# Performance work log

Measured on AMD Instinct MI355X. Metric: run time of the kernel, lower is better.

The kernel has to match this reference:

```python
import jax, jax.numpy as jnp
import numpy as np

RADIUS = 0.5
NEG_INF = -jnp.inf


def setup_inputs() -> dict:
    key = jax.random.key(0)
    ks = jax.random.split(key, 10)
    N_q, N_o, pos_dim, latent_dim = 2048, 2048, 3, 64
    enc_dim = 3 * pos_dim  # q_pos, o_pos, rel
    inp = {
        "h_obs": jax.random.normal(ks[0], (N_o, latent_dim), dtype=jnp.float32),
        "x_obs": jax.random.normal(ks[1], (N_o, latent_dim), dtype=jnp.float32),
        "pos_obs": jax.random.uniform(ks[2], (N_o, pos_dim), dtype=jnp.float32),
        "pos_query": jax.random.uniform(ks[3], (N_q, pos_dim), dtype=jnp.float32),
        # kernel_mlp: Linear(enc_dim->latent) + ReLU + Linear(latent->1)
        "W1": jax.random.normal(ks[4], (enc_dim, latent_dim), dtype=jnp.float32) / np.sqrt(enc_dim),
        "b1": jnp.zeros((latent_dim,), dtype=jnp.float32),
        "W2": jax.random.normal(ks[5], (latent_dim, 1), dtype=jnp.float32) / np.sqrt(latent_dim),
        "b2": jnp.zeros((1,), dtype=jnp.float32),
        # value_proj: Linear(latent->latent)
        "Wv": jax.random.normal(ks[6], (latent_dim, latent_dim), dtype=jnp.float32) / np.sqrt(latent_dim),
        "bv": jnp.zeros((latent_dim,), dtype=jnp.float32),
    }
    return inp


def reference(h_obs, x_obs, pos_obs, pos_query, W1, b1, W2, b2, Wv, bv):
    # rel: [N_q, N_o, pos_dim]
    rel = pos_query[:, None, :] - pos_obs[None, :, :]
    N_q, N_o, _ = rel.shape
    pos_q_exp = jnp.broadcast_to(pos_query[:, None, :], rel.shape)
    pos_o_exp = jnp.broadcast_to(pos_obs[None, :, :], rel.shape)
    kernel_input = jnp.concatenate([pos_q_exp, pos_o_exp, rel], axis=-1)  # [N_q, N_o, 3*pos_dim]
    # small pointwise MLP over all pairs
    hidden = jax.nn.relu(jnp.einsum('qoe,el->qol', kernel_input, W1) + b1)  # [N_q, N_o, latent]
    logits = jnp.einsum('qol,lk->qok', hidden, W2)[..., 0] + b2[0]          # [N_q, N_o]
    # radius mask
    dist = jnp.linalg.norm(rel, axis=-1)
    logits = jnp.where(dist > RADIUS, NEG_INF, logits)
    # softmax over observations (dim=1)
    weights = jax.nn.softmax(logits, axis=1)  # [N_q, N_o]
    v = h_obs @ Wv + bv                        # [N_o, latent]
    h_query = weights @ v                      # [N_q, latent]
    return h_query
```

## Files before the change

### kernel.cpp

```cpp
#include <hip/hip_runtime.h>

#define NQ 2048
#define NO 2048
#define NOC 32

constexpr size_t OFF_PH = 0;
constexpr size_t OFF_PS = (size_t)NOC * NQ * 64;

__global__ __launch_bounds__(256, 4) void gano_main(
    const float* __restrict__ h_obs,
    const float* __restrict__ pos_obs,
    const float* __restrict__ pos_query,
    const float* __restrict__ W1,
    const float* __restrict__ b1,
    const float* __restrict__ W2,
    float* __restrict__ Ph,
    float* __restrict__ Ps)
{
    __shared__ __align__(16) float tl[64 * 68];
    __shared__ __align__(16) float ue[16 * 64 * 4];
    __shared__ float w1q[3 * 64];
    __shared__ float w1o[3 * 64];
    __shared__ float b1l[64];
    __shared__ __align__(16) float w2l[64];
    __shared__ float po[3 * 64];
    __shared__ float sbuf[4 * 64];

    const int tid  = threadIdx.x;
    const int lane = tid & 63;
    const int wave = __builtin_amdgcn_readfirstlane(tid >> 6);
    const int qg = blockIdx.x >> 5;
    const int oc = blockIdx.x & 31;
    const int obase = oc * 64;
    const int q = qg * 64 + lane;

    if (tid < 64) {
        float w6 = W1[6 * 64 + tid], w7 = W1[7 * 64 + tid], w8 = W1[8 * 64 + tid];
        w1q[0 * 64 + tid] = W1[0 * 64 + tid] + w6;
        w1q[1 * 64 + tid] = W1[1 * 64 + tid] + w7;
        w1q[2 * 64 + tid] = W1[2 * 64 + tid] + w8;
        w1o[0 * 64 + tid] = W1[3 * 64 + tid] - w6;
        w1o[1 * 64 + tid] = W1[4 * 64 + tid] - w7;
        w1o[2 * 64 + tid] = W1[5 * 64 + tid] - w8;
        b1l[tid] = b1[tid];
        w2l[tid] = W2[tid];
    }
    float pq0 = pos_query[q * 3 + 0];
    float pq1 = pos_query[q * 3 + 1];
    float pq2 = pos_query[q * 3 + 2];
    float po0 = pos_obs[(obase + lane) * 3 + 0];
    float po1 = pos_obs[(obase + lane) * 3 + 1];
    float po2 = pos_obs[(obase + lane) * 3 + 2];
    if (wave == 0) { po[lane] = po0; po[64 + lane] = po1; po[128 + lane] = po2; }
    __syncthreads();

#pragma unroll
    for (int j = 0; j < 16; ++j) {
        int l = wave * 16 + j;
        tl[l * 68 + lane] = po0 * w1o[l] + po1 * w1o[64 + l] + po2 * w1o[128 + l];
    }
#pragma unroll
    for (int k = 0; k < 4; ++k) {
        int lb = wave * 4 + k;
        float4 uv;
        {
            int l = lb * 4;
            uv.x = b1l[l+0] + pq0 * w1q[l+0] + pq1 * w1q[64 + l+0] + pq2 * w1q[128 + l+0];
            uv.y = b1l[l+1] + pq0 * w1q[l+1] + pq1 * w1q[64 + l+1] + pq2 * w1q[128 + l+1];
            uv.z = b1l[l+2] + pq0 * w1q[l+2] + pq1 * w1q[64 + l+2] + pq2 * w1q[128 + l+2];
            uv.w = b1l[l+3] + pq0 * w1q[l+3] + pq1 * w1q[64 + l+3] + pq2 * w1q[128 + l+3];
        }
        *(float4*)(ue + (size_t)(lb * 64 + lane) * 4) = uv;
    }
    __syncthreads();

    float lg[16];
#pragma unroll
    for (int o = 0; o < 16; ++o) lg[o] = 0.f;
    const int ow = wave * 16;
#pragma unroll
    for (int lb = 0; lb < 16; ++lb) {
        float4 u4 = *(const float4*)(ue + (size_t)(lb * 64 + lane) * 4);
        float4 w4 = *(const float4*)(w2l + lb * 4);
#pragma unroll
        for (int dl = 0; dl < 4; ++dl) {
            const int l = lb * 4 + dl;
            const float4* tr = (const float4*)(tl + l * 68 + ow);
            float ul = (dl == 0) ? u4.x : (dl == 1) ? u4.y : (dl == 2) ? u4.z : u4.w;
            float wl = (dl == 0) ? w4.x : (dl == 1) ? w4.y : (dl == 2) ? w4.z : w4.w;
#pragma unroll
            for (int j = 0; j < 4; ++j) {
                float4 t4 = tr[j];
                lg[4 * j + 0] += wl * fmaxf(ul + t4.x, 0.f);
                lg[4 * j + 1] += wl * fmaxf(ul + t4.y, 0.f);
                lg[4 * j + 2] += wl * fmaxf(ul + t4.z, 0.f);
                lg[4 * j + 3] += wl * fmaxf(ul + t4.w, 0.f);
            }
        }
    }
    float e[16], spart = 0.f;
#pragma unroll
    for (int o = 0; o < 16; ++o) {
        float d0 = pq0 - po[ow + o];
        float d1 = pq1 - po[64 + ow + o];
        float d2 = pq2 - po[128 + ow + o];
        float dd = d0 * d0 + d1 * d1 + d2 * d2;
        float ev = (dd > 0.25f) ? 0.f : __expf(lg[o]);
        e[o] = ev; spart += ev;
    }
    __syncthreads();
#pragma unroll
    for (int o = 0; o < 16; ++o) ue[(size_t)(ow + o) * 64 + lane] = e[o];
    sbuf[wave * 64 + lane] = spart;
    __syncthreads();

    float h0 = 0.f, h1 = 0.f, h2 = 0.f, h3 = 0.f, h4 = 0.f, h5 = 0.f, h6 = 0.f, h7 = 0.f;
    float h8 = 0.f, h9 = 0.f, hA = 0.f, hB = 0.f, hC = 0.f, hD = 0.f, hE = 0.f, hF = 0.f;
    const float* vb = h_obs + (size_t)obase * 64 + ow;
#pragma unroll 4
    for (int o = 0; o < 64; ++o) {
        float eo = ue[(size_t)o * 64 + lane];
        const float4* vr = (const float4*)(vb + (size_t)o * 64);
        float4 v0 = vr[0], v1 = vr[1], v2 = vr[2], v3 = vr[3];
        h0 += eo * v0.x; h1 += eo * v0.y; h2 += eo * v0.z; h3 += eo * v0.w;
        h4 += eo * v1.x; h5 += eo * v1.y; h6 += eo * v1.z; h7 += eo * v1.w;
        h8 += eo * v2.x; h9 += eo * v2.y; hA += eo * v2.z; hB += eo * v2.w;
        hC += eo * v3.x; hD += eo * v3.y; hE += eo * v3.z; hF += eo * v3.w;
    }

    float* hp = Ph + ((size_t)oc * NQ + (size_t)qg * 64 + lane) * 64 + ow;
    ((float4*)hp)[0] = make_float4(h0, h1, h2, h3);
    ((float4*)hp)[1] = make_float4(h4, h5, h6, h7);
    ((float4*)hp)[2] = make_float4(h8, h9, hA, hB);
    ((float4*)hp)[3] = make_float4(hC, hD, hE, hF);
    if (wave == 0) {
        float s = sbuf[lane] + sbuf[64 + lane] + sbuf[128 + lane] + sbuf[192 + lane];
        Ps[(size_t)oc * NQ + (size_t)qg * 64 + lane] = s;
    }
}

__global__ __launch_bounds__(256, 2) void gano_comb(
    const float* __restrict__ Ph,
    const float* __restrict__ Ps,
    const float* __restrict__ Wv,
    const float* __restrict__ bv,
    float* __restrict__ out)
{
    __shared__ __align__(16) float wv[64 * 64];
    __shared__ __align__(16) float g[4 * 68];
    const int tid  = threadIdx.x;
    const int lane = tid & 63;
    const int wave = tid >> 6;
    const int q0 = blockIdx.x * 4;
    {
        const float4* src = (const float4*)Wv;
        float4* dst = (float4*)wv;
#pragma unroll
        for (int k = 0; k < 4; ++k) dst[tid + k * 256] = src[tid + k * 256];
    }
    {
        const int qi = wave, k = lane;
        float acc = 0.f;
#pragma unroll
        for (int c = 0; c < NOC; ++c)
            acc += Ph[((size_t)c * NQ + q0 + qi) * 64 + k];
        g[qi * 68 + k] = acc;
        if (k == 0) {
            float ss = 0.f;
#pragma unroll
            for (int c = 0; c < NOC; ++c) ss += Ps[(size_t)c * NQ + q0 + qi];
            g[qi * 68 + 64] = ss;
        }
    }
    __syncthreads();
    const float* gq = g + wave * 68;
    float inv = 1.0f / gq[64];
    float a0 = 0.f, a1 = 0.f, a2 = 0.f, a3 = 0.f;
#pragma unroll
    for (int kb = 0; kb < 16; ++kb) {
        float4 g4 = *(const float4*)(gq + kb * 4);
        a0 += g4.x * wv[(kb * 4 + 0) * 64 + lane];
        a1 += g4.y * wv[(kb * 4 + 1) * 64 + lane];
        a2 += g4.z * wv[(kb * 4 + 2) * 64 + lane];
        a3 += g4.w * wv[(kb * 4 + 3) * 64 + lane];
    }
    out[(size_t)(q0 + wave) * 64 + lane] = ((a0 + a1) + (a2 + a3)) * inv + bv[lane];
}

extern "C" void kernel_launch(void* const* d_in, const int* in_sizes, int n_in,
                              void* d_out, int out_size, void* d_ws, size_t ws_size,
                              hipStream_t stream) {
    const float* h_obs     = (const float*)d_in[0];
    const float* pos_obs   = (const float*)d_in[2];
    const float* pos_query = (const float*)d_in[3];
    const float* W1        = (const float*)d_in[4];
    const float* b1        = (const float*)d_in[5];
    const float* W2        = (const float*)d_in[6];
    const float* Wv        = (const float*)d_in[8];
    const float* bv        = (const float*)d_in[9];
    float* ws  = (float*)d_ws;
    float* out = (float*)d_out;

    gano_main<<<dim3(1024), dim3(256), 0, stream>>>(h_obs, pos_obs, pos_query, W1, b1, W2,
                                                    ws + OFF_PH, ws + OFF_PS);
    gano_comb<<<dim3(NQ / 4), dim3(256), 0, stream>>>(ws + OFF_PH, ws + OFF_PS, Wv, bv, out);
}
```

Measured before the change: 108.2 us.

## Precompute obs-side hidden term in prep kernel and read via scalar loads

Adds a prep kernel that computes the observation-side first-layer term T[o][l] once into workspace, instead of every block rebuilding it in LDS. The main kernel keeps the query-side hidden vector in 64 registers and reads T rows, W2, pos_obs and h_obs through wave-uniform (readfirstlane) addresses, so those loads can become scalar loads rather than LDS traffic. Most LDS staging and several barriers are removed. The costs are an extra kernel launch, much higher register pressure from the u[64] array, which may hurt occupancy under launch_bounds(256,4), and dependence on scalar-cache bandwidth.

```diff
diff --git a/kernel.cpp b/kernel.cpp
--- a/kernel.cpp
+++ b/kernel.cpp
@@ -4,10 +4,25 @@
 #define NO 2048
 #define NOC 32
 
-constexpr size_t OFF_PH = 0;
-constexpr size_t OFF_PS = (size_t)NOC * NQ * 64;
+constexpr size_t OFF_T  = 0;
+constexpr size_t OFF_PH = (size_t)NO * 64;
+constexpr size_t OFF_PS = OFF_PH + (size_t)NOC * NQ * 64;
+
+__global__ __launch_bounds__(256) void gano_prep(
+    const float* __restrict__ pos_obs,
+    const float* __restrict__ W1,
+    float* __restrict__ T)
+{
+    int gid = blockIdx.x * 256 + threadIdx.x;
+    int o = gid >> 6, l = gid & 63;
+    float po0 = pos_obs[o * 3 + 0], po1 = pos_obs[o * 3 + 1], po2 = pos_obs[o * 3 + 2];
+    float w3 = W1[3 * 64 + l], w4 = W1[4 * 64 + l], w5 = W1[5 * 64 + l];
+    float w6 = W1[6 * 64 + l], w7 = W1[7 * 64 + l], w8 = W1[8 * 64 + l];
+    T[(size_t)o * 64 + l] = po0 * (w3 - w6) + po1 * (w4 - w7) + po2 * (w5 - w8);
+}
 
 __global__ __launch_bounds__(256, 4) void gano_main(
+    const float* __restrict__ T,
     const float* __restrict__ h_obs,
     const float* __restrict__ pos_obs,
     const float* __restrict__ pos_query,
@@ -17,13 +32,7 @@
     float* __restrict__ Ph,
     float* __restrict__ Ps)
 {
-    __shared__ __align__(16) float tl[64 * 68];
-    __shared__ __align__(16) float ue[16 * 64 * 4];
-    __shared__ float w1q[3 * 64];
-    __shared__ float w1o[3 * 64];
-    __shared__ float b1l[64];
-    __shared__ __align__(16) float w2l[64];
-    __shared__ float po[3 * 64];
+    __shared__ float ue[64 * 64];
     __shared__ float sbuf[4 * 64];
 
     const int tid  = threadIdx.x;
@@ -32,100 +41,63 @@
     const int qg = blockIdx.x >> 5;
     const int oc = blockIdx.x & 31;
     const int obase = oc * 64;
-    const int q = qg * 64 + lane;
+    const int q  = qg * 64 + lane;
+    const int ow = wave * 16;
 
-    if (tid < 64) {
-        float w6 = W1[6 * 64 + tid], w7 = W1[7 * 64 + tid], w8 = W1[8 * 64 + tid];
-        w1q[0 * 64 + tid] = W1[0 * 64 + tid] + w6;
-        w1q[1 * 64 + tid] = W1[1 * 64 + tid] + w7;
-        w1q[2 * 64 + tid] = W1[2 * 64 + tid] + w8;
-        w1o[0 * 64 + tid] = W1[3 * 64 + tid] - w6;
-        w1o[1 * 64 + tid] = W1[4 * 64 + tid] - w7;
-        w1o[2 * 64 + tid] = W1[5 * 64 + tid] - w8;
-        b1l[tid] = b1[tid];
-        w2l[tid] = W2[tid];
-    }
     float pq0 = pos_query[q * 3 + 0];
     float pq1 = pos_query[q * 3 + 1];
     float pq2 = pos_query[q * 3 + 2];
-    float po0 = pos_obs[(obase + lane) * 3 + 0];
-    float po1 = pos_obs[(obase + lane) * 3 + 1];
-    float po2 = pos_obs[(obase + lane) * 3 + 2];
-    if (wave == 0) { po[lane] = po0; po[64 + lane] = po1; po[128 + lane] = po2; }
-    __syncthreads();
 
+    float u[64];
 #pragma unroll
-    for (int j = 0; j < 16; ++j) {
-        int l = wave * 16 + j;
-        tl[l * 68 + lane] = po0 * w1o[l] + po1 * w1o[64 + l] + po2 * w1o[128 + l];
+    for (int l = 0; l < 64; ++l) {
+        float a = b1[l];
+        a += pq0 * W1[0 * 64 + l];
+        a += pq1 * W1[1 * 64 + l];
+        a += pq2 * W1[2 * 64 + l];
+        a += pq0 * W1[6 * 64 + l];
+        a += pq1 * W1[7 * 64 + l];
+        a += pq2 * W1[8 * 64 + l];
+        u[l] = a;
     }
+
+    float spart = 0.f;
+#pragma unroll 2
+    for (int o = 0; o < 16; ++o) {
+        const int toff = __builtin_amdgcn_readfirstlane((obase + ow + o) * 64);
+        const float* __restrict__ trow = T + toff;
+        float a0 = 0.f, a1 = 0.f, a2 = 0.f, a3 = 0.f;
 #pragma unroll
-    for (int k = 0; k < 4; ++k) {
-        int lb = wave * 4 + k;
-        float4 uv;
-        {
-            int l = lb * 4;
-            uv.x = b1l[l+0] + pq0 * w1q[l+0] + pq1 * w1q[64 + l+0] + pq2 * w1q[128 + l+0];
-            uv.y = b1l[l+1] + pq0 * w1q[l+1] + pq1 * w1q[64 + l+1] + pq2 * w1q[128 + l+1];
-            uv.z = b1l[l+2] + pq0 * w1q[l+2] + pq1 * w1q[64 + l+2] + pq2 * w1q[128 + l+2];
-            uv.w = b1l[l+3] + pq0 * w1q[l+3] + pq1 * w1q[64 + l+3] + pq2 * w1q[128 + l+3];
+        for (int l = 0; l < 64; l += 4) {
+            a0 += W2[l + 0] * fmaxf(u[l + 0] + trow[l + 0], 0.f);
+            a1 += W2[l + 1] * fmaxf(u[l + 1] + trow[l + 1], 0.f);
+            a2 += W2[l + 2] * fmaxf(u[l + 2] + trow[l + 2], 0.f);
+            a3 += W2[l + 3] * fmaxf(u[l + 3] + trow[l + 3], 0.f);
         }
-        *(float4*)(ue + (size_t)(lb * 64 + lane) * 4) = uv;
+        float lgo = (a0 + a1) + (a2 + a3);
+        const int poff = __builtin_amdgcn_readfirstlane((obase + ow + o) * 3);
+        float d0 = pq0 - pos_obs[poff + 0];
+        float d1 = pq1 - pos_obs[poff + 1];
+        float d2 = pq2 - pos_obs[poff + 2];
+        float dd = d0 * d0 + d1 * d1 + d2 * d2;
+        float ev = (dd > 0.25f) ? 0.f : __expf(lgo);
+        spart += ev;
+        ue[(ow + o) * 64 + lane] = ev;
     }
-    __syncthreads();
-
-    float lg[16];
-#pragma unroll
-    for (int o = 0; o < 16; ++o) lg[o] = 0.f;
-    const int ow = wave * 16;
-#pragma unroll
-    for (int lb = 0; lb < 16; ++lb) {
-        float4 u4 = *(const float4*)(ue + (size_t)(lb * 64 + lane) * 4);
-        float4 w4 = *(const float4*)(w2l + lb * 4);
-#pragma unroll
-        for (int dl = 0; dl < 4; ++dl) {
-            const int l = lb * 4 + dl;
-            const float4* tr = (const float4*)(tl + l * 68 + ow);
-            float ul = (dl == 0) ? u4.x : (dl == 1) ? u4.y : (dl == 2) ? u4.z : u4.w;
-            float wl = (dl == 0) ? w4.x : (dl == 1) ? w4.y : (dl == 2) ? w4.z : w4.w;
-#pragma unroll
-            for (int j = 0; j < 4; ++j) {
-                float4 t4 = tr[j];
-                lg[4 * j + 0] += wl * fmaxf(ul + t4.x, 0.f);
-                lg[4 * j + 1] += wl * fmaxf(ul + t4.y, 0.f);
-                lg[4 * j + 2] += wl * fmaxf(ul + t4.z, 0.f);
-                lg[4 * j + 3] += wl * fmaxf(ul + t4.w, 0.f);
-            }
-        }
-    }
-    float e[16], spart = 0.f;
-#pragma unroll
-    for (int o = 0; o < 16; ++o) {
-        float d0 = pq0 - po[ow + o];
-        float d1 = pq1 - po[64 + ow + o];
-        float d2 = pq2 - po[128 + ow + o];
-        float dd = d0 * d0 + d1 * d1 + d2 * d2;
-        float ev = (dd > 0.25f) ? 0.f : __expf(lg[o]);
-        e[o] = ev; spart += ev;
-    }
-    __syncthreads();
-#pragma unroll
-    for (int o = 0; o < 16; ++o) ue[(size_t)(ow + o) * 64 + lane] = e[o];
     sbuf[wave * 64 + lane] = spart;
     __syncthreads();
 
     float h0 = 0.f, h1 = 0.f, h2 = 0.f, h3 = 0.f, h4 = 0.f, h5 = 0.f, h6 = 0.f, h7 = 0.f;
     float h8 = 0.f, h9 = 0.f, hA = 0.f, hB = 0.f, hC = 0.f, hD = 0.f, hE = 0.f, hF = 0.f;
-    const float* vb = h_obs + (size_t)obase * 64 + ow;
-#pragma unroll 4
+#pragma unroll 2
     for (int o = 0; o < 64; ++o) {
-        float eo = ue[(size_t)o * 64 + lane];
-        const float4* vr = (const float4*)(vb + (size_t)o * 64);
-        float4 v0 = vr[0], v1 = vr[1], v2 = vr[2], v3 = vr[3];
-        h0 += eo * v0.x; h1 += eo * v0.y; h2 += eo * v0.z; h3 += eo * v0.w;
-        h4 += eo * v1.x; h5 += eo * v1.y; h6 += eo * v1.z; h7 += eo * v1.w;
-        h8 += eo * v2.x; h9 += eo * v2.y; hA += eo * v2.z; hB += eo * v2.w;
-        hC += eo * v3.x; hD += eo * v3.y; hE += eo * v3.z; hF += eo * v3.w;
+        float eo = ue[o * 64 + lane];
+        const int hoff = __builtin_amdgcn_readfirstlane((obase + o) * 64 + ow);
+        const float* __restrict__ hr = h_obs + hoff;
+        h0 += eo * hr[0];  h1 += eo * hr[1];  h2 += eo * hr[2];  h3 += eo * hr[3];
+        h4 += eo * hr[4];  h5 += eo * hr[5];  h6 += eo * hr[6];  h7 += eo * hr[7];
+        h8 += eo * hr[8];  h9 += eo * hr[9];  hA += eo * hr[10]; hB += eo * hr[11];
+        hC += eo * hr[12]; hD += eo * hr[13]; hE += eo * hr[14]; hF += eo * hr[15];
     }
 
     float* hp = Ph + ((size_t)oc * NQ + (size_t)qg * 64 + lane) * 64 + ow;
@@ -201,7 +173,8 @@
     float* ws  = (float*)d_ws;
     float* out = (float*)d_out;
 
-    gano_main<<<dim3(1024), dim3(256), 0, stream>>>(h_obs, pos_obs, pos_query, W1, b1, W2,
-                                                    ws + OFF_PH, ws + OFF_PS);
+    gano_prep<<<dim3(NO * 64 / 256), dim3(256), 0, stream>>>(pos_obs, W1, ws + OFF_T);
+    gano_main<<<dim3(1024), dim3(256), 0, stream>>>(ws + OFF_T, h_obs, pos_obs, pos_query,
+                                                    W1, b1, W2, ws + OFF_PH, ws + OFF_PS);
     gano_comb<<<dim3(NQ / 4), dim3(256), 0, stream>>>(ws + OFF_PH, ws + OFF_PS, Wv, bv, out);
 }
```

Measured after the change: 120.8 us. 11.6% more time.
